# Kernel optimization log

Hardware: AMD Instinct MI355X
Metric: run time of the kernel (lower is better)

Reference implementation:

```python
import jax, jax.numpy as jnp
import numpy as np
import math

B, S, HID, H = 8, 512, 1024, 16
D = HID // H
ATT_SPAN = 512  # max_position_embeddings


def setup_inputs() -> dict:
    key = jax.random.key(0)
    ks = jax.random.split(key, 12)
    sd = 0.02
    hidden_states = jax.random.normal(ks[0], (B, S, HID), jnp.float32)
    attention_mask = jnp.zeros((B, 1, 1, S), jnp.float32)
    # DeBERTa build_relative_position: rel[i, j] = i - j, shape [1, 1, S, S]
    rel = (jnp.arange(S)[:, None] - jnp.arange(S)[None, :]).astype(jnp.int32)
    relative_pos = rel[None, None]
    Wq = jax.random.normal(ks[1], (HID, HID), jnp.float32) * sd
    bq = jnp.zeros((HID,), jnp.float32)
    Wk = jax.random.normal(ks[2], (HID, HID), jnp.float32) * sd
    bk = jnp.zeros((HID,), jnp.float32)
    Wv = jax.random.normal(ks[3], (HID, HID), jnp.float32) * sd
    bv = jnp.zeros((HID,), jnp.float32)
    Wpk = jax.random.normal(ks[4], (HID, HID), jnp.float32) * sd
    bpk = jnp.zeros((HID,), jnp.float32)
    rel_emb = jax.random.normal(ks[5], (2 * ATT_SPAN, HID), jnp.float32) * sd
    return dict(hidden_states=hidden_states, attention_mask=attention_mask,
                relative_pos=relative_pos, Wq=Wq, bq=bq, Wk=Wk, bk=bk,
                Wv=Wv, bv=bv, Wpk=Wpk, bpk=bpk, rel_emb=rel_emb)


def _fwd(hidden_states, attention_mask, relative_pos, Wq, bq, Wk, bk, Wv, bv, Wpk, bpk, rel_emb):
    b, s, _ = hidden_states.shape

    def proj(x, W, bias):  # [b,s,hid] -> [b,h,s,d]
        return (x @ W.T + bias).reshape(b, s, H, D).transpose(0, 2, 1, 3)

    q = proj(hidden_states, Wq, bq)
    k = proj(hidden_states, Wk, bk)
    v = proj(hidden_states, Wv, bv)

    # content-to-content scores, scaled by sqrt(3*num_heads) as in source
    s_content = jnp.einsum('bhid,bhjd->bhij', q, k) / math.sqrt(3.0 * H)

    # positional projections (source uses pos_key layer for BOTH key and query)
    # rel_emb: [2*ATT_SPAN, HID] -> [H, 2*ATT_SPAN, D]
    pos = (rel_emb @ Wpk.T + bpk).reshape(2 * ATT_SPAN, H, D).transpose(1, 0, 2)

    # c2p: q @ pos^T / sqrt(all_head_size * 3), then gather along last axis
    c2p_full = jnp.einsum('bhid,hpd->bhip', q, pos) / math.sqrt(HID * 3.0)  # [b,h,s,2P]
    c2p_pos = jnp.clip(relative_pos + ATT_SPAN, 0, 2 * ATT_SPAN - 1)
    c2p_pos = jnp.broadcast_to(c2p_pos, (b, H, s, s)).astype(jnp.int32)
    c2p = jnp.take_along_axis(c2p_full, c2p_pos, axis=-1)  # [b,h,s,s]

    # p2c: pos / sqrt(3*H) @ k^T, gather along dim -2 with same index
    p2c_full = jnp.einsum('hpd,bhjd->bhpj', pos / math.sqrt(3.0 * H), k)  # [b,h,2P,s]
    p2c = jnp.take_along_axis(p2c_full, c2p_pos, axis=-2)  # [b,h,s,s]

    score = s_content + c2p + p2c + attention_mask
    probs = jax.nn.softmax(score, axis=-1)  # dropout is identity in eval
    out = jnp.einsum('bhij,bhjd->bhid', probs, v)
    return out.transpose(0, 2, 1, 3).reshape(b, s, HID)


def reference(hidden_states, attention_mask, relative_pos, Wq, bq, Wk, bk, Wv, bv, Wpk, bpk, rel_emb):
    return _fwd(hidden_states, attention_mask, relative_pos, Wq, bq, Wk, bk, Wv, bv, Wpk, bpk, rel_emb)
```

## Files before the change

kernel.cpp:

```cpp
#include <hip/hip_runtime.h>
#include <cstdint>
#include <cstddef>

static constexpr int NB  = 8;
static constexpr int S   = 512;
static constexpr int HID = 1024;
static constexpr int NH  = 16;
static constexpr int DH  = 64;
static constexpr int P2  = 1024;

static constexpr float INV_S1 = 0.14433756729740643f;

typedef __bf16 v8bf  __attribute__((ext_vector_type(8)));
typedef __bf16 v4bf  __attribute__((ext_vector_type(4)));
typedef float  f32x4 __attribute__((ext_vector_type(4)));

#define MFMA16(acc, a, b) acc = __builtin_amdgcn_mfma_f32_16x16x32_bf16(a, b, acc, 0, 0, 0)

#define GLOAD_LDS16(gp, lp) __builtin_amdgcn_global_load_lds( \
    (const __attribute__((address_space(1))) void*)(gp), \
    (__attribute__((address_space(3))) void*)(lp), 16, 0, 0)

__global__ void castall(const float* __restrict__ x,  const float* __restrict__ wq,
                        const float* __restrict__ wk, const float* __restrict__ wv,
                        const float* __restrict__ wpk, const float* __restrict__ rel,
                        __bf16* __restrict__ ob) {
  size_t e = ((size_t)blockIdx.x * 256 + threadIdx.x) * 4;
  if (e >= 9437184) return;
  const float* src; size_t off;
  if (e < 4194304) { src = x; off = e; }
  else {
    int r = (int)((e - 4194304) >> 20);
    off = (e - 4194304) & 1048575;
    src = (r == 0) ? wq : (r == 1) ? wk : (r == 2) ? wv : (r == 3) ? wpk : rel;
  }
  float4 v = *(const float4*)(src + off);
  v4bf o;
  o[0] = (__bf16)v.x; o[1] = (__bf16)v.y; o[2] = (__bf16)v.z; o[3] = (__bf16)v.w;
  *(v4bf*)(ob + e) = o;
}

__launch_bounds__(256, 4)
__global__ void proj_gemm(const __bf16* __restrict__ Xb, const __bf16* __restrict__ Rb,
                          const __bf16* __restrict__ Wqb, const __bf16* __restrict__ Wkb,
                          const __bf16* __restrict__ Wvb, const __bf16* __restrict__ Wpkb,
                          const float* __restrict__ bq, const float* __restrict__ bk_,
                          const float* __restrict__ bv_, const float* __restrict__ bpk,
                          __bf16* __restrict__ qo, __bf16* __restrict__ ko,
                          __bf16* __restrict__ vto, __bf16* __restrict__ po) {
  const int z = blockIdx.z;
  const __bf16* A; const __bf16* W; const float* bias; __bf16* out; int M; float osc;
  if      (z == 0) { A = Xb; W = Wqb;  bias = bq;  out = qo;  M = 4096; osc = INV_S1; }
  else if (z == 1) { A = Xb; W = Wkb;  bias = bk_; out = ko;  M = 4096; osc = 1.0f; }
  else if (z == 2) { A = Xb; W = Wvb;  bias = bv_; out = vto; M = 4096; osc = 1.0f; }
  else             { A = Rb; W = Wpkb; bias = bpk; out = po;  M = 1024; osc = INV_S1; }
  const int m0 = blockIdx.x * 128;
  if (m0 >= M) return;
  const int n0 = blockIdx.y * 128;
  const int K = 1024;

  __shared__ __bf16 Al[128 * 64];
  __shared__ __bf16 Bl[128 * 64];

  const int t = threadIdx.x;
  const int w = t >> 6, lane = t & 63, q4 = lane >> 4, cc = lane & 15;
  const int wm = w >> 1, wn = w & 1;
  const int srow_in = lane >> 3;
  const int sseg    = ((lane & 7) ^ srow_in) * 8;

  f32x4 acc[4][4] = {};

  for (int k0 = 0; k0 < K; k0 += 64) {
    __syncthreads();
    #pragma unroll
    for (int i = 0; i < 4; i++) {
      int rr = w * 32 + i * 8;
      int gr = rr + srow_in;
      GLOAD_LDS16(&A[(size_t)(m0 + gr) * K + k0 + sseg], &Al[rr * 64]);
      GLOAD_LDS16(&W[(size_t)(n0 + gr) * K + k0 + sseg], &Bl[rr * 64]);
    }
    __syncthreads();
    #pragma unroll
    for (int kk = 0; kk < 2; kk++) {
      v8bf af[4], bfg[4];
      const int phys = ((4 * kk + q4) ^ (cc & 7)) * 8;
      #pragma unroll
      for (int mt = 0; mt < 4; mt++)
        af[mt] = *(const v8bf*)(&Al[(wm * 64 + mt * 16 + cc) * 64 + phys]);
      #pragma unroll
      for (int nt = 0; nt < 4; nt++)
        bfg[nt] = *(const v8bf*)(&Bl[(wn * 64 + nt * 16 + cc) * 64 + phys]);
      #pragma unroll
      for (int mt = 0; mt < 4; mt++)
        #pragma unroll
        for (int nt = 0; nt < 4; nt++)
          MFMA16(acc[mt][nt], af[mt], bfg[nt]);
    }
  }

  #pragma unroll
  for (int mt = 0; mt < 4; mt++) {
    #pragma unroll
    for (int nt = 0; nt < 4; nt++) {
      int n = n0 + wn * 64 + nt * 16 + cc;
      float bsv = bias[n];
      if (z == 2) {
        int m_base = m0 + wm * 64 + mt * 16 + q4 * 4;
        int bb = m_base >> 9, ss = m_base & 511, hh = n >> 6, dd = n & 63;
        v4bf st;
        st[0] = (__bf16)(acc[mt][nt][0] + bsv);
        st[1] = (__bf16)(acc[mt][nt][1] + bsv);
        st[2] = (__bf16)(acc[mt][nt][2] + bsv);
        st[3] = (__bf16)(acc[mt][nt][3] + bsv);
        *(v4bf*)(&out[(((size_t)bb * 16 + hh) * 64 + dd) * 512 + ss]) = st;
      } else {
        #pragma unroll
        for (int r = 0; r < 4; r++) {
          int m = m0 + wm * 64 + mt * 16 + q4 * 4 + r;
          float val = (acc[mt][nt][r] + bsv) * osc;
          size_t idx;
          if (z < 2)
            idx = ((size_t)(m >> 9) * 16 + (n >> 6)) * (512 * 64) + (size_t)(m & 511) * 64 + (n & 63);
          else
            idx = (size_t)(n >> 6) * (1024 * 64) + (size_t)m * 64 + (n & 63);
          out[idx] = (__bf16)val;
        }
      }
    }
  }
}

__launch_bounds__(256, 4)
__global__ void attn(const __bf16* __restrict__ qb, const __bf16* __restrict__ kb,
                     const __bf16* __restrict__ vtb, const __bf16* __restrict__ posb,
                     const float* __restrict__ mask,
                     __bf16* __restrict__ Op, float2* __restrict__ lm) {
  const int bh = blockIdx.y, b = bh >> 4, h = bh & 15;
  const int i0 = blockIdx.x * 64;
  const int jh = blockIdx.z;

  __shared__ __bf16 Sb[64 * 136];

  const int t = threadIdx.x, w = t >> 6, lane = t & 63, q4 = lane >> 4, cc = lane & 15;
  const int arow = w * 16;
  const size_t bho = (size_t)bh * (S * DH);
  const __bf16* qp  = qb  + bho;
  const __bf16* kp  = kb  + bho;
  const __bf16* vtp = vtb + bho;
  const __bf16* pp  = posb + (size_t)h * (P2 * DH);

  v8bf aq0 = *(const v8bf*)(&qp[(size_t)(i0 + arow + cc) * DH + q4 * 8]);
  v8bf aq1 = *(const v8bf*)(&qp[(size_t)(i0 + arow + cc) * DH + 32 + q4 * 8]);

  f32x4 Oc[4] = {};
  float mrow[4], lrow[4];
  #pragma unroll
  for (int r = 0; r < 4; r++) { mrow[r] = -__builtin_inff(); lrow[r] = 0.f; }

#define LDP(d0, d1, U) { int p_ = pw0 + 16 * (U) + cc; p_ = min(max(p_, 0), P2 - 1); \
  const __bf16* pr_ = &pp[(size_t)p_ * DH + q4 * 8]; \
  d0 = *(const v8bf*)pr_; d1 = *(const v8bf*)(pr_ + 32); }
#define LDK(d0, d1, NT) { const __bf16* kr_ = &kp[(size_t)(j0 + (NT) * 16 + cc) * DH + q4 * 8]; \
  d0 = *(const v8bf*)kr_; d1 = *(const v8bf*)(kr_ + 32); }
#define GT(U, P0, P1) { f32x4 g_ = {}; MFMA16(g_, aq0, P0); MFMA16(g_, aq1, P1); \
  _Pragma("unroll") for (int r_ = 0; r_ < 4; r_++) { \
    int jj_ = q4 * 4 + r_ - 16 * (U) - cc + 63; \
    if ((unsigned)jj_ < 64u) Sb[(arow + q4 * 4 + r_) * 136 + jj_ * 2] = (__bf16)(g_[r_] * 0.8660254f); } }
#define HT(U, NT, P0, P1, K0, K1) { f32x4 h_ = {}; MFMA16(h_, P0, K0); MFMA16(h_, P1, K1); \
  _Pragma("unroll") for (int r_ = 0; r_ < 4; r_++) { \
    int ar_ = 16 * (U) + q4 * 4 + r_ + 16 * (NT) + cc - 63; \
    if ((unsigned)ar_ < 16u) Sb[(arow + ar_) * 136 + (16 * (NT) + cc) * 2 + 1] = (__bf16)h_[r_]; } }
#define CT(NT, K0, K1) { f32x4 c_ = {}; MFMA16(c_, aq0, K0); MFMA16(c_, aq1, K1); accc[NT] = c_; }

  for (int jt = jh * 4; jt < jh * 4 + 4; jt++) {
    const int j0 = jt * 64;
    const int pw0 = i0 + arow - j0 + 449;

    float mk[4];
    #pragma unroll
    for (int nt = 0; nt < 4; nt++) mk[nt] = mask[(size_t)b * S + j0 + nt * 16 + cc];

    f32x4 accc[4];
    v8bf p40,p41,p30,p31,p20,p21,p10,p11,p00,p01;
    v8bf k00,k01,k10,k11,k20,k21,k30,k31;

    LDP(p40, p41, 4); LDK(k00, k01, 0);
    LDP(p30, p31, 3); LDK(k10, k11, 1);
    GT(4, p40, p41); HT(4, 0, p40, p41, k00, k01); CT(0, k00, k01);
    LDP(p20, p21, 2); LDK(k20, k21, 2);
    GT(3, p30, p31); HT(3, 0, p30, p31, k00, k01); HT(3, 1, p30, p31, k10, k11); CT(1, k10, k11);
    LDP(p10, p11, 1); LDK(k30, k31, 3);
    GT(2, p20, p21); HT(2, 1, p20, p21, k10, k11); HT(2, 2, p20, p21, k20, k21); CT(2, k20, k21);
    LDP(p00, p01, 0);
    GT(1, p10, p11); HT(1, 2, p10, p11, k20, k21); HT(1, 3, p10, p11, k30, k31); CT(3, k30, k31);
    GT(0, p00, p01); HT(0, 3, p00, p01, k30, k31);

    float sc[4][4];
    float tmax[4] = { -__builtin_inff(), -__builtin_inff(), -__builtin_inff(), -__builtin_inff() };
    #pragma unroll
    for (int nt = 0; nt < 4; nt++) {
      int jj = nt * 16 + cc;
      #pragma unroll
      for (int r = 0; r < 4; r++) {
        const __bf16* slot = &Sb[(arow + q4 * 4 + r) * 136 + jj * 2];
        float s = accc[nt][r] + (float)slot[0] + (float)slot[1] + mk[nt];
        sc[nt][r] = s;
        tmax[r] = fmaxf(tmax[r], s);
      }
    }
    #pragma unroll
    for (int off = 1; off < 16; off <<= 1)
      #pragma unroll
      for (int r = 0; r < 4; r++) tmax[r] = fmaxf(tmax[r], __shfl_xor(tmax[r], off, 64));

    v8bf vf[2][4];
    #pragma unroll
    for (int kk = 0; kk < 2; kk++)
      #pragma unroll
      for (int dt = 0; dt < 4; dt++)
        vf[kk][dt] = *(const v8bf*)(&vtp[(size_t)(dt * 16 + cc) * S + j0 + kk * 32 + q4 * 8]);

    float alpha[4], psum[4];
    #pragma unroll
    for (int r = 0; r < 4; r++) {
      float mnew = fmaxf(mrow[r], tmax[r]);
      alpha[r] = __expf(mrow[r] - mnew);
      mrow[r] = mnew;
      psum[r] = 0.f;
    }
    #pragma unroll
    for (int nt = 0; nt < 4; nt++)
      #pragma unroll
      for (int r = 0; r < 4; r++) {
        float p = __expf(sc[nt][r] - mrow[r]);
        psum[r] += p;
        Sb[(arow + q4 * 4 + r) * 136 + nt * 16 + cc] = (__bf16)p;
      }
    #pragma unroll
    for (int off = 1; off < 16; off <<= 1)
      #pragma unroll
      for (int r = 0; r < 4; r++) psum[r] += __shfl_xor(psum[r], off, 64);
    #pragma unroll
    for (int r = 0; r < 4; r++) lrow[r] = lrow[r] * alpha[r] + psum[r];
    #pragma unroll
    for (int dt = 0; dt < 4; dt++)
      #pragma unroll
      for (int r = 0; r < 4; r++) Oc[dt][r] *= alpha[r];

    #pragma unroll
    for (int kk = 0; kk < 2; kk++) {
      v8bf ap = *(const v8bf*)(&Sb[(arow + cc) * 136 + kk * 32 + q4 * 8]);
      #pragma unroll
      for (int dt = 0; dt < 4; dt++)
        MFMA16(Oc[dt], ap, vf[kk][dt]);
    }
  }

  const size_t plane = (size_t)jh * (128 * S);
  #pragma unroll
  for (int r = 0; r < 4; r++) {
    int i = i0 + arow + q4 * 4 + r;
    float rl = 1.0f / lrow[r];
    if (cc == 0) lm[plane + (size_t)bh * S + i] = make_float2(mrow[r], lrow[r]);
    #pragma unroll
    for (int dt = 0; dt < 4; dt++)
      Op[(plane + (size_t)bh * S + i) * 64 + dt * 16 + cc] = (__bf16)(Oc[dt][r] * rl);
  }
#undef LDP
#undef LDK
#undef GT
#undef HT
#undef CT
}

__global__ void combine(const __bf16* __restrict__ Op, const float2* __restrict__ lm,
                        float* __restrict__ out) {
  int tg = blockIdx.x * 256 + threadIdx.x;
  int gi = tg >> 4;
  int d4 = (tg & 15) * 4;
  int bh = gi >> 9, i = gi & 511, b = bh >> 4, h = bh & 15;
  float2 a = lm[gi];
  float2 c = lm[65536 + gi];
  float mmax = fmaxf(a.x, c.x);
  float w0 = __expf(a.x - mmax) * a.y;
  float w1 = __expf(c.x - mmax) * c.y;
  float inv = 1.0f / (w0 + w1);
  w0 *= inv; w1 *= inv;
  v4bf o0 = *(const v4bf*)(&Op[(size_t)gi * 64 + d4]);
  v4bf o1 = *(const v4bf*)(&Op[(size_t)(4194304) + (size_t)gi * 64 + d4]);
  float4 res;
  res.x = w0 * (float)o0[0] + w1 * (float)o1[0];
  res.y = w0 * (float)o0[1] + w1 * (float)o1[1];
  res.z = w0 * (float)o0[2] + w1 * (float)o1[2];
  res.w = w0 * (float)o0[3] + w1 * (float)o1[3];
  *(float4*)(&out[((size_t)b * S + i) * HID + h * 64 + d4]) = res;
}

extern "C" void kernel_launch(void* const* d_in, const int* in_sizes, int n_in,
                              void* d_out, int out_size, void* d_ws, size_t ws_size,
                              hipStream_t stream) {
  const float* hs   = (const float*)d_in[0];
  const float* mask = (const float*)d_in[1];
  const float* Wq  = (const float*)d_in[3];
  const float* bq  = (const float*)d_in[4];
  const float* Wk  = (const float*)d_in[5];
  const float* bk  = (const float*)d_in[6];
  const float* Wv  = (const float*)d_in[7];
  const float* bv  = (const float*)d_in[8];
  const float* Wpk = (const float*)d_in[9];
  const float* bpk = (const float*)d_in[10];
  const float* rel = (const float*)d_in[11];
  float* out = (float*)d_out;

  char* ws = (char*)d_ws;
  __bf16* cb   = (__bf16*)ws;
  __bf16* Xb   = cb;
  __bf16* Wqb  = cb + 4194304;
  __bf16* Wkb  = cb + 5242880;
  __bf16* Wvb  = cb + 6291456;
  __bf16* Wpkb = cb + 7340032;
  __bf16* Rb   = cb + 8388608;
  __bf16* qb   = (__bf16*)(ws + 18874368);
  __bf16* kb   = (__bf16*)(ws + 27262976);
  __bf16* vtb  = (__bf16*)(ws + 35651584);
  __bf16* posb = (__bf16*)(ws + 44040192);
  __bf16* Op   = (__bf16*)ws;
  float2* lm   = (float2*)(ws + 16777216);

  castall<<<9216, 256, 0, stream>>>(hs, Wq, Wk, Wv, Wpk, rel, cb);

  proj_gemm<<<dim3(32, 8, 4), 256, 0, stream>>>(Xb, Rb, Wqb, Wkb, Wvb, Wpkb,
                                                bq, bk, bv, bpk, qb, kb, vtb, posb);

  attn<<<dim3(8, 128, 2), 256, 0, stream>>>(qb, kb, vtb, posb, mask, Op, lm);

  combine<<<4096, 256, 0, stream>>>(Op, lm, out);
}
```

Baseline: 252.7 us.

## Drop split-KV attention and combine kernel; write final output directly

```diff
diff --git a/kernel.cpp b/kernel.cpp
--- a/kernel.cpp
+++ b/kernel.cpp
@@ -134,10 +134,9 @@
 __global__ void attn(const __bf16* __restrict__ qb, const __bf16* __restrict__ kb,
                      const __bf16* __restrict__ vtb, const __bf16* __restrict__ posb,
                      const float* __restrict__ mask,
-                     __bf16* __restrict__ Op, float2* __restrict__ lm) {
+                     float* __restrict__ out) {
   const int bh = blockIdx.y, b = bh >> 4, h = bh & 15;
   const int i0 = blockIdx.x * 64;
-  const int jh = blockIdx.z;
 
   __shared__ __bf16 Sb[64 * 136];
 
@@ -172,7 +171,7 @@
     if ((unsigned)ar_ < 16u) Sb[(arow + ar_) * 136 + (16 * (NT) + cc) * 2 + 1] = (__bf16)h_[r_]; } }
 #define CT(NT, K0, K1) { f32x4 c_ = {}; MFMA16(c_, aq0, K0); MFMA16(c_, aq1, K1); accc[NT] = c_; }
 
-  for (int jt = jh * 4; jt < jh * 4 + 4; jt++) {
+  for (int jt = 0; jt < 8; jt++) {
     const int j0 = jt * 64;
     const int pw0 = i0 + arow - j0 + 449;
 
@@ -256,44 +255,20 @@
     }
   }
 
-  const size_t plane = (size_t)jh * (128 * S);
   #pragma unroll
   for (int r = 0; r < 4; r++) {
     int i = i0 + arow + q4 * 4 + r;
     float rl = 1.0f / lrow[r];
-    if (cc == 0) lm[plane + (size_t)bh * S + i] = make_float2(mrow[r], lrow[r]);
+    float* orow = &out[((size_t)b * S + i) * HID + h * 64];
     #pragma unroll
     for (int dt = 0; dt < 4; dt++)
-      Op[(plane + (size_t)bh * S + i) * 64 + dt * 16 + cc] = (__bf16)(Oc[dt][r] * rl);
+      orow[dt * 16 + cc] = Oc[dt][r] * rl;
   }
 #undef LDP
 #undef LDK
 #undef GT
 #undef HT
 #undef CT
-}
-
-__global__ void combine(const __bf16* __restrict__ Op, const float2* __restrict__ lm,
-                        float* __restrict__ out) {
-  int tg = blockIdx.x * 256 + threadIdx.x;
-  int gi = tg >> 4;
-  int d4 = (tg & 15) * 4;
-  int bh = gi >> 9, i = gi & 511, b = bh >> 4, h = bh & 15;
-  float2 a = lm[gi];
-  float2 c = lm[65536 + gi];
-  float mmax = fmaxf(a.x, c.x);
-  float w0 = __expf(a.x - mmax) * a.y;
-  float w1 = __expf(c.x - mmax) * c.y;
-  float inv = 1.0f / (w0 + w1);
-  w0 *= inv; w1 *= inv;
-  v4bf o0 = *(const v4bf*)(&Op[(size_t)gi * 64 + d4]);
-  v4bf o1 = *(const v4bf*)(&Op[(size_t)(4194304) + (size_t)gi * 64 + d4]);
-  float4 res;
-  res.x = w0 * (float)o0[0] + w1 * (float)o1[0];
-  res.y = w0 * (float)o0[1] + w1 * (float)o1[1];
-  res.z = w0 * (float)o0[2] + w1 * (float)o1[2];
-  res.w = w0 * (float)o0[3] + w1 * (float)o1[3];
-  *(float4*)(&out[((size_t)b * S + i) * HID + h * 64 + d4]) = res;
 }
 
 extern "C" void kernel_launch(void* const* d_in, const int* in_sizes, int n_in,
@@ -324,15 +299,11 @@
   __bf16* kb   = (__bf16*)(ws + 27262976);
   __bf16* vtb  = (__bf16*)(ws + 35651584);
   __bf16* posb = (__bf16*)(ws + 44040192);
-  __bf16* Op   = (__bf16*)ws;
-  float2* lm   = (float2*)(ws + 16777216);
 
   castall<<<9216, 256, 0, stream>>>(hs, Wq, Wk, Wv, Wpk, rel, cb);
 
   proj_gemm<<<dim3(32, 8, 4), 256, 0, stream>>>(Xb, Rb, Wqb, Wkb, Wvb, Wpkb,
                                                 bq, bk, bv, bpk, qb, kb, vtb, posb);
 
-  attn<<<dim3(8, 128, 2), 256, 0, stream>>>(qb, kb, vtb, posb, mask, Op, lm);
-
-  combine<<<4096, 256, 0, stream>>>(Op, lm, out);
+  attn<<<dim3(8, 128), 256, 0, stream>>>(qb, kb, vtb, posb, mask, out);
 }
```

Result: no change. 248.8 us (-1.5%).
